# Kernel optimization log

Measured on AMD Instinct MI355X. Metric: run time of the kernel, lower is better.

The kernel has to match this reference:

```python
import jax, jax.numpy as jnp
import numpy as np

G, M, K = 4096, 50, 30          # graphs, nodes per graph, sort-pool k
H, NUM_LAYERS, F_IN = 32, 3, 128
DEG = 8
N = G * M
E = N * DEG
D_LAT = H * NUM_LAYERS + 1       # 97 = conv1d kernel/stride
DENSE_DIM = (((K - 2) // 2 + 1) - 5 + 1) * 32  # 352


def setup_inputs() -> dict:
    key = jax.random.key(0)
    ks = jax.random.split(key, 14)
    x = jax.random.normal(ks[0], (N, F_IN), dtype=jnp.float32)
    # graph-local random edges so each subgraph is self-contained
    offs = (jnp.arange(E, dtype=jnp.int32) // (M * DEG)) * M
    src = jax.random.randint(ks[1], (E,), 0, M, dtype=jnp.int32) + offs
    dst = jax.random.randint(ks[2], (E,), 0, M, dtype=jnp.int32) + offs
    edge_index = jnp.stack([src, dst])
    batch = jnp.repeat(jnp.arange(G, dtype=jnp.int32), M)

    def lin(k, i, o):
        return (jax.random.normal(k, (i, o), dtype=jnp.float32) / np.sqrt(i)).astype(jnp.float32)

    W0, b0 = lin(ks[3], F_IN, H), jnp.zeros((H,), jnp.float32)
    W1, b1 = lin(ks[4], H, H), jnp.zeros((H,), jnp.float32)
    W2, b2 = lin(ks[5], H, H), jnp.zeros((H,), jnp.float32)
    W3, b3 = lin(ks[6], H, 1), jnp.zeros((1,), jnp.float32)
    C1w = (jax.random.normal(ks[7], (16, 1, D_LAT)) / np.sqrt(D_LAT)).astype(jnp.float32)
    C1b = jnp.zeros((16,), jnp.float32)
    C2w = (jax.random.normal(ks[8], (32, 16, 5)) / np.sqrt(16 * 5)).astype(jnp.float32)
    C2b = jnp.zeros((32,), jnp.float32)
    L1w, L1b = lin(ks[9], DENSE_DIM, 128), jnp.zeros((128,), jnp.float32)
    L2w, L2b = lin(ks[10], 128, 1), jnp.zeros((1,), jnp.float32)
    return {"x": x, "edge_index": edge_index, "batch": batch,
            "W0": W0, "b0": b0, "W1": W1, "b1": b1, "W2": W2, "b2": b2,
            "W3": W3, "b3": b3, "C1w": C1w, "C1b": C1b, "C2w": C2w, "C2b": C2b,
            "L1w": L1w, "L1b": L1b, "L2w": L2w, "L2b": L2b}


def _gcn_norm(edge_index, n):
    # add self loops, symmetric normalization (PyG GCNConv default)
    loop = jnp.arange(n, dtype=edge_index.dtype)
    src = jnp.concatenate([edge_index[0], loop])
    dst = jnp.concatenate([edge_index[1], loop])
    deg = jax.ops.segment_sum(jnp.ones_like(dst, dtype=jnp.float32), dst, num_segments=n)
    dinv = jnp.where(deg > 0, deg ** -0.5, 0.0)
    return src, dst, dinv[src] * dinv[dst]


def _gcn_conv(h, W, b, src, dst, norm, n):
    h = h @ W                                    # [N, out]
    msg = h[src] * norm[:, None]                 # gather + weight
    return jax.ops.segment_sum(msg, dst, num_segments=n) + b


def reference(x, edge_index, batch, W0, b0, W1, b1, W2, b2, W3, b3,
              C1w, C1b, C2w, C2b, L1w, L1b, L2w, L2b):
    n = x.shape[0]
    src, dst, norm = _gcn_norm(edge_index, n)
    h1 = jnp.tanh(_gcn_conv(x, W0, b0, src, dst, norm, n))
    h2 = jnp.tanh(_gcn_conv(h1, W1, b1, src, dst, norm, n))
    h3 = jnp.tanh(_gcn_conv(h2, W2, b2, src, dst, norm, n))
    h4 = jnp.tanh(_gcn_conv(h3, W3, b3, src, dst, norm, n))
    lat = jnp.concatenate([h1, h2, h3, h4], axis=-1)      # [N, 97]
    # global_sort_pool: graphs are contiguous equal-size blocks (batch = arange(G).repeat(M)),
    # sort nodes within each graph by last channel, descending, keep top K
    xd = lat.reshape(G, M, D_LAT)
    order = jnp.argsort(-xd[..., -1], axis=1)             # [G, M]
    xs = jnp.take_along_axis(xd, order[..., None], axis=1)[:, :K]  # [G, K, 97]
    # Conv1d(1,16,97,stride=97) on [G,1,K*97] == per-slot linear over the 97 latent dims
    z = jnp.einsum('gtd,cd->gct', xs, C1w[:, 0, :]) + C1b[None, :, None]  # [G,16,K]
    z = jax.nn.relu(z)
    z = z.reshape(G, 16, K // 2, 2).max(axis=-1)          # MaxPool1d(2,2) -> [G,16,15]
    z = jax.lax.conv_general_dilated(z, C2w, window_strides=(1,), padding='VALID',
                                     dimension_numbers=('NCH', 'OIH', 'NCH'))
    z = jax.nn.relu(z + C2b[None, :, None])               # [G,32,11]
    z = z.reshape(G, -1)                                  # [G,352]
    z = jax.nn.relu(z @ L1w + L1b)
    # dropout: eval mode (identity)
    return z @ L2w + L2b                                  # [G,1]
```

## Files before the change

kernel.cpp:

```cpp
#include <hip/hip_runtime.h>
#include <math.h>

#define NG 4096
#define M 50
#define KTOP 30
#define H 32
#define F_IN 128
#define EPG 400
#define PADE 552
#define E_TOTAL (NG * EPG)
#define DLAT 97
#define LATS 100
#define NTHREADS 256
#define WS_C1P 0
#define XH 64

__device__ __forceinline__ float fast_tanh(float x) {
    x = fminf(fmaxf(x, -15.f), 15.f);
    float e = __expf(2.f * x);
    return 1.f - 2.f / (e + 1.f);
}

__global__ void prep_kernel(const float* __restrict__ C1w, float* __restrict__ ws) {
    const int tid = blockIdx.x * blockDim.x + threadIdx.x;
    if (tid < 1600) {
        int c = tid / 100, d = tid - c * 100;
        ws[WS_C1P + tid] = (d < DLAT) ? C1w[c * DLAT + d] : 0.f;
    }
}

template <int KIN>
__device__ __forceinline__ void gcn_matmul_acc(const float* hin, int istride,
                                               const float* W,
                                               const int* rows, float* acc, int j) {
#pragma unroll 2
    for (int k4 = 0; k4 < KIN / 4; k4++) {
        const float w0 = W[(4 * k4 + 0) * H + j];
        const float w1 = W[(4 * k4 + 1) * H + j];
        const float w2 = W[(4 * k4 + 2) * H + j];
        const float w3 = W[(4 * k4 + 3) * H + j];
#pragma unroll
        for (int r = 0; r < 7; r++) {
            const float4 xv = *(const float4*)(hin + rows[r] * istride + 4 * k4);
            acc[r] += xv.x * w0 + xv.y * w1 + xv.z * w2 + xv.w * w3;
        }
    }
}

template <int KIN>
__device__ __forceinline__ void gcn_matmul(const float* hin, int istride,
                                           const float* W,
                                           float (*tb)[H], const float* dinv, int tid) {
    const int j = tid & 31, iset = tid >> 5;
    float acc[7];
    int rows[7];
#pragma unroll
    for (int r = 0; r < 7; r++) {
        acc[r] = 0.f;
        int i = iset + r * 8;
        rows[r] = (i >= M) ? (M - 1) : i;
    }
    gcn_matmul_acc<KIN>(hin, istride, W, rows, acc, j);
#pragma unroll
    for (int r = 0; r < 7; r++) {
        int i = iset + r * 8;
        if (i < M) tb[i][j] = acc[r] * dinv[i];
    }
}

__device__ __forceinline__ void gcn_agg(const float (*tbuf)[H], const float* __restrict__ b,
                                        float (*lat)[LATS], int col0,
                                        const float* dinv, const unsigned short* csr_off,
                                        const unsigned char* csr_src, int tid) {
    const int j = tid & 31, iset = tid >> 5;
    for (int i = iset; i < M; i += 8) {
        float acc = tbuf[i][j];
        int e0 = csr_off[i], e1 = csr_off[i + 1];
        for (int e = e0; e < e1; e += 4) {
            unsigned sp = *(const unsigned*)(csr_src + e);
            acc += tbuf[sp & 255][j];
            acc += tbuf[(sp >> 8) & 255][j];
            acc += tbuf[(sp >> 16) & 255][j];
            acc += tbuf[sp >> 24][j];
        }
        lat[i][col0 + j] = fast_tanh(acc * dinv[i] + b[j]);
    }
}

struct Post {
    float pbuf[16][15];
    union {
        struct { float z1[16][KTOP]; unsigned char ord[52]; } a;
        struct { float z2[352]; float red[256]; } b;
    } u;
};

__global__ __launch_bounds__(NTHREADS, 4)
void dgcnn_kernel(const float* __restrict__ x, const int* __restrict__ eidx,
                  const float* __restrict__ ws,
                  const float* __restrict__ W0, const float* __restrict__ b0,
                  const float* __restrict__ W1, const float* __restrict__ b1,
                  const float* __restrict__ W2, const float* __restrict__ b2,
                  const float* __restrict__ W3, const float* __restrict__ b3,
                  const float* __restrict__ C1b,
                  const float* __restrict__ C2w, const float* __restrict__ C2b,
                  const float* __restrict__ L1w, const float* __restrict__ L1b,
                  const float* __restrict__ L2w, const float* __restrict__ L2b,
                  float* __restrict__ out) {
    __shared__ __align__(16) union Big {
        struct { float xs[M][XH]; float w0h[XH][H]; } p1;
        float lat[M][LATS];
    } big;
    __shared__ __align__(16) union TP {
        float tbuf[M + 1][H];
        Post post;
    } tp;
    __shared__ __align__(16) union W12U {
        float w[2][H][H];
        float c2w[32 * 16 * 5];
    } w12u;
    __shared__ unsigned char csr_src[PADE];
    __shared__ unsigned short csr_off[M + 2];
    __shared__ int   degi[M];
    __shared__ float dinv[M];

    const int g = blockIdx.x;
    const int tid = threadIdx.x;
    const int nbase = g * M;
    const int ebase = g * EPG;

    {
        const float4* xg4 = (const float4*)(x + (size_t)nbase * F_IN);
        float4* xs4 = (float4*)big.p1.xs;
        for (int idx = tid; idx < M * XH / 4; idx += NTHREADS) {
            int i = idx >> 4, q = idx & 15;
            xs4[idx] = xg4[i * 32 + q];
        }
        float4* w0f = (float4*)big.p1.w0h;
        const float4* w0g = (const float4*)W0;
        for (int idx = tid; idx < 512; idx += NTHREADS)
            w0f[idx] = w0g[idx];
        float4* wf = (float4*)w12u.w;
        for (int idx = tid; idx < 512; idx += NTHREADS) {
            const float4* srcp = (idx < 256) ? ((const float4*)W1 + idx)
                                             : ((const float4*)W2 + (idx - 256));
            wf[idx] = *srcp;
        }
    }
    if (tid < M) degi[tid] = 1;
    for (int idx = tid; idx < PADE / 4; idx += NTHREADS)
        ((unsigned*)csr_src)[idx] = 0x32323232u;
    __syncthreads();
    for (int e = tid; e < EPG; e += NTHREADS) {
        int d = eidx[E_TOTAL + ebase + e] - nbase;
        atomicAdd(&degi[d], 1);
    }
    __syncthreads();
    if (tid < M) dinv[tid] = rsqrtf((float)degi[tid]);
    if (tid < 64) {
        int cnt  = (tid < M) ? (degi[tid] - 1) : 0;
        int cntp = (cnt + 3) & ~3;
        int incl = cntp;
#pragma unroll
        for (int off = 1; off < 64; off <<= 1) {
            int nv = __shfl_up(incl, off);
            if (tid >= off) incl += nv;
        }
        if (tid < M) {
            csr_off[tid] = (unsigned short)(incl - cntp);
            degi[tid] = incl - cntp;
        }
        if (tid == M - 1) csr_off[M] = (unsigned short)incl;
    }
    __syncthreads();
    const int j1 = tid & 31, iset1 = tid >> 5;
    float acc1[7];
    int rows1[7];
#pragma unroll
    for (int r = 0; r < 7; r++) {
        acc1[r] = 0.f;
        int i = iset1 + r * 8;
        rows1[r] = (i >= M) ? (M - 1) : i;
    }
    for (int e = tid; e < EPG; e += NTHREADS) {
        int s = eidx[ebase + e] - nbase;
        int d = eidx[E_TOTAL + ebase + e] - nbase;
        int pos = atomicAdd(&degi[d], 1);
        csr_src[pos] = (unsigned char)s;
    }
    gcn_matmul_acc<XH>(&big.p1.xs[0][0], XH, &big.p1.w0h[0][0], rows1, acc1, j1);
    __syncthreads();
    {
        const float4* xg4 = (const float4*)(x + (size_t)nbase * F_IN);
        float4* xs4 = (float4*)big.p1.xs;
        for (int idx = tid; idx < M * XH / 4; idx += NTHREADS) {
            int i = idx >> 4, q = idx & 15;
            xs4[idx] = xg4[i * 32 + 16 + q];
        }
        float4* w0f = (float4*)big.p1.w0h;
        const float4* w0g = (const float4*)(W0 + XH * H);
        for (int idx = tid; idx < 512; idx += NTHREADS)
            w0f[idx] = w0g[idx];
    }
    __syncthreads();
    gcn_matmul_acc<XH>(&big.p1.xs[0][0], XH, &big.p1.w0h[0][0], rows1, acc1, j1);
#pragma unroll
    for (int r = 0; r < 7; r++) {
        int i = iset1 + r * 8;
        if (i < M) tp.tbuf[i][j1] = acc1[r] * dinv[i];
    }
    if (tid < H) tp.tbuf[M][tid] = 0.f;
    __syncthreads();

    gcn_agg(tp.tbuf, b0, big.lat, 0, dinv, csr_off, csr_src, tid);
    for (int idx = tid; idx < 3 * M; idx += NTHREADS)
        big.lat[idx / 3][DLAT + idx % 3] = 0.f;
    __syncthreads();
    gcn_matmul<H>(&big.lat[0][0], LATS, &w12u.w[0][0][0], tp.tbuf, dinv, tid);
    __syncthreads();
    gcn_agg(tp.tbuf, b1, big.lat, 32, dinv, csr_off, csr_src, tid);
    __syncthreads();
    gcn_matmul<H>(&big.lat[0][32], LATS, &w12u.w[1][0][0], tp.tbuf, dinv, tid);
    __syncthreads();
    gcn_agg(tp.tbuf, b2, big.lat, 64, dinv, csr_off, csr_src, tid);
    {
        float4* cf = (float4*)w12u.c2w;
        const float4* cg = (const float4*)C2w;
        for (int idx = tid; idx < 640; idx += NTHREADS)
            cf[idx] = cg[idx];
    }
    __syncthreads();
    if (tid < M) {
        float acc = 0.f;
        for (int k = 0; k < H; k++) acc += big.lat[tid][64 + k] * W3[k];
        tp.tbuf[tid][0] = acc * dinv[tid];
    }
    __syncthreads();
    if (tid < M) {
        float acc = tp.tbuf[tid][0];
        int e0 = csr_off[tid], e1 = csr_off[tid + 1];
        for (int e = e0; e < e1; e += 4) {
            unsigned sp = *(const unsigned*)(csr_src + e);
            acc += tp.tbuf[sp & 255][0] + tp.tbuf[(sp >> 8) & 255][0]
                 + tp.tbuf[(sp >> 16) & 255][0] + tp.tbuf[sp >> 24][0];
        }
        big.lat[tid][96] = tanhf(acc * dinv[tid] + b3[0]);
    }
    __syncthreads();

    if (tid < M) {
        float v = big.lat[tid][96];
        int r = 0;
        for (int jj = 0; jj < M; jj++) {
            float vj = big.lat[jj][96];
            r += (vj > v) || (vj == v && jj < tid);
        }
        tp.post.u.a.ord[r] = (unsigned char)tid;
    }
    __syncthreads();

    for (int idx = tid; idx < 16 * KTOP; idx += NTHREADS) {
        int t = idx >> 4, c = idx & 15;
        const float4* row = (const float4*)big.lat[tp.post.u.a.ord[t]];
        const float4* cw  = (const float4*)(ws + WS_C1P + c * LATS);
        float acc = 0.f;
#pragma unroll 5
        for (int q = 0; q < LATS / 4; q++) {
            float4 rv = row[q], wv = cw[q];
            acc += rv.x * wv.x + rv.y * wv.y + rv.z * wv.z + rv.w * wv.w;
        }
        tp.post.u.a.z1[c][t] = fmaxf(acc + C1b[c], 0.f);
    }
    __syncthreads();

    for (int idx = tid; idx < 16 * 15; idx += NTHREADS) {
        int c = idx / 15, t = idx - c * 15;
        tp.post.pbuf[c][t] = fmaxf(tp.post.u.a.z1[c][2 * t],
                                   tp.post.u.a.z1[c][2 * t + 1]);
    }
    __syncthreads();

    for (int idx = tid; idx < 352; idx += NTHREADS) {
        int o = idx / 11, t = idx - o * 11;
        float acc = C2b[o];
        for (int i = 0; i < 16; i++) {
#pragma unroll
            for (int k = 0; k < 5; k++)
                acc += tp.post.pbuf[i][t + k] * w12u.c2w[(o * 16 + i) * 5 + k];
        }
        tp.post.u.b.z2[idx] = fmaxf(acc, 0.f);
    }
    __syncthreads();

    {
        int jj = tid & 127, half = tid >> 7;
        int f0 = half * 176;
        const float* Lp = L1w + (size_t)f0 * 128 + jj;
        const float* zp = tp.post.u.b.z2 + f0;
        float a0 = 0.f, a1 = 0.f, a2 = 0.f, a3 = 0.f;
#pragma unroll 2
        for (int f = 0; f < 176; f += 4) {
            a0 += zp[f]     * Lp[(f)     * 128];
            a1 += zp[f + 1] * Lp[(f + 1) * 128];
            a2 += zp[f + 2] * Lp[(f + 2) * 128];
            a3 += zp[f + 3] * Lp[(f + 3) * 128];
        }
        float acc = (a0 + a1) + (a2 + a3) + ((half == 0) ? L1b[jj] : 0.f);
        tp.post.u.b.red[tid] = acc;
    }
    __syncthreads();
    if (tid < 128)
        tp.post.u.b.red[tid] =
            fmaxf(tp.post.u.b.red[tid] + tp.post.u.b.red[tid + 128], 0.f)
            * L2w[tid];
    __syncthreads();
    if (tid < 64) {
        float v = tp.post.u.b.red[tid] + tp.post.u.b.red[tid + 64];
#pragma unroll
        for (int off = 32; off >= 1; off >>= 1)
            v += __shfl_down(v, off);
        if (tid == 0) out[g] = v + L2b[0];
    }
}

extern "C" void kernel_launch(void* const* d_in, const int* in_sizes, int n_in,
                              void* d_out, int out_size, void* d_ws, size_t ws_size,
                              hipStream_t stream) {
    const float* x    = (const float*)d_in[0];
    const int*   eidx = (const int*)d_in[1];
    float* ws = (float*)d_ws;
    prep_kernel<<<7, 256, 0, stream>>>((const float*)d_in[11], ws);
    dgcnn_kernel<<<NG, NTHREADS, 0, stream>>>(
        x, eidx, ws,
        (const float*)d_in[3],  (const float*)d_in[4],
        (const float*)d_in[5],  (const float*)d_in[6],
        (const float*)d_in[7],  (const float*)d_in[8],
        (const float*)d_in[9],  (const float*)d_in[10],
        (const float*)d_in[12],
        (const float*)d_in[13], (const float*)d_in[14],
        (const float*)d_in[15], (const float*)d_in[16],
        (const float*)d_in[17], (const float*)d_in[18],
        (float*)d_out);
}
```

Before: 361.4 us.

## Transpose GCN weights in LDS and use packed FP32 FMA for matmuls

Weights W0, W1 and W2 are now stored transposed in shared memory with padded strides, so each thread reads contiguous pairs of its output column. The inner products use v_pk_fma_f32 via inline asm, carrying two partial sums per row. The matmul regions also raise wave priority with s_setprio. Conv1 uses packed FMA and conv2 splits its accumulation into two chains. The intent is to halve FMA issue count and cut LDS load instructions, at the cost of more bank-sensitive transposed stores, an extra reduction, and changed summation order.

```diff
diff --git a/kernel.cpp b/kernel.cpp
--- a/kernel.cpp
+++ b/kernel.cpp
@@ -14,6 +14,16 @@
 #define NTHREADS 256
 #define WS_C1P 0
 #define XH 64
+#define W0TS 66
+#define W12TS 34
+
+typedef float f32x2 __attribute__((ext_vector_type(2)));
+
+__device__ __forceinline__ f32x2 pk_fma(f32x2 a, f32x2 b, f32x2 c) {
+    f32x2 d;
+    asm("v_pk_fma_f32 %0, %1, %2, %3" : "=v"(d) : "v"(a), "v"(b), "v"(c));
+    return d;
+}
 
 __device__ __forceinline__ float fast_tanh(float x) {
     x = fminf(fmaxf(x, -15.f), 15.f);
@@ -31,40 +41,41 @@
 
 template <int KIN>
 __device__ __forceinline__ void gcn_matmul_acc(const float* hin, int istride,
-                                               const float* W,
-                                               const int* rows, float* acc, int j) {
+                                               const float* wtj,
+                                               const int* rows, f32x2* acc2) {
 #pragma unroll 2
     for (int k4 = 0; k4 < KIN / 4; k4++) {
-        const float w0 = W[(4 * k4 + 0) * H + j];
-        const float w1 = W[(4 * k4 + 1) * H + j];
-        const float w2 = W[(4 * k4 + 2) * H + j];
-        const float w3 = W[(4 * k4 + 3) * H + j];
+        const f32x2 wA = *(const f32x2*)(wtj + 4 * k4);
+        const f32x2 wB = *(const f32x2*)(wtj + 4 * k4 + 2);
 #pragma unroll
         for (int r = 0; r < 7; r++) {
-            const float4 xv = *(const float4*)(hin + rows[r] * istride + 4 * k4);
-            acc[r] += xv.x * w0 + xv.y * w1 + xv.z * w2 + xv.w * w3;
+            const f32x2* xp = (const f32x2*)(hin + rows[r] * istride + 4 * k4);
+            acc2[r] = pk_fma(xp[0], wA, acc2[r]);
+            acc2[r] = pk_fma(xp[1], wB, acc2[r]);
         }
     }
 }
 
 template <int KIN>
 __device__ __forceinline__ void gcn_matmul(const float* hin, int istride,
-                                           const float* W,
+                                           const float* wtj,
                                            float (*tb)[H], const float* dinv, int tid) {
     const int j = tid & 31, iset = tid >> 5;
-    float acc[7];
+    f32x2 acc[7];
     int rows[7];
 #pragma unroll
     for (int r = 0; r < 7; r++) {
-        acc[r] = 0.f;
+        acc[r] = (f32x2){0.f, 0.f};
         int i = iset + r * 8;
         rows[r] = (i >= M) ? (M - 1) : i;
     }
-    gcn_matmul_acc<KIN>(hin, istride, W, rows, acc, j);
+    __builtin_amdgcn_s_setprio(1);
+    gcn_matmul_acc<KIN>(hin, istride, wtj, rows, acc);
+    __builtin_amdgcn_s_setprio(0);
 #pragma unroll
     for (int r = 0; r < 7; r++) {
         int i = iset + r * 8;
-        if (i < M) tb[i][j] = acc[r] * dinv[i];
+        if (i < M) tb[i][j] = (acc[r].x + acc[r].y) * dinv[i];
     }
 }
 
@@ -108,7 +119,7 @@
                   const float* __restrict__ L2w, const float* __restrict__ L2b,
                   float* __restrict__ out) {
     __shared__ __align__(16) union Big {
-        struct { float xs[M][XH]; float w0h[XH][H]; } p1;
+        struct { float xs[M][XH]; float w0t[H][W0TS]; } p1;
         float lat[M][LATS];
     } big;
     __shared__ __align__(16) union TP {
@@ -116,7 +127,7 @@
         Post post;
     } tp;
     __shared__ __align__(16) union W12U {
-        float w[2][H][H];
+        float w[2][H][W12TS];
         float c2w[32 * 16 * 5];
     } w12u;
     __shared__ unsigned char csr_src[PADE];
@@ -136,15 +147,19 @@
             int i = idx >> 4, q = idx & 15;
             xs4[idx] = xg4[i * 32 + q];
         }
-        float4* w0f = (float4*)big.p1.w0h;
         const float4* w0g = (const float4*)W0;
-        for (int idx = tid; idx < 512; idx += NTHREADS)
-            w0f[idx] = w0g[idx];
-        float4* wf = (float4*)w12u.w;
         for (int idx = tid; idx < 512; idx += NTHREADS) {
-            const float4* srcp = (idx < 256) ? ((const float4*)W1 + idx)
-                                             : ((const float4*)W2 + (idx - 256));
-            wf[idx] = *srcp;
+            int k = idx >> 3, q4 = (idx & 7) * 4;
+            float4 v = w0g[idx];
+            big.p1.w0t[q4 + 0][k] = v.x; big.p1.w0t[q4 + 1][k] = v.y;
+            big.p1.w0t[q4 + 2][k] = v.z; big.p1.w0t[q4 + 3][k] = v.w;
+        }
+        for (int idx = tid; idx < 512; idx += NTHREADS) {
+            int m = idx >> 8, r = idx & 255;
+            int k = r >> 3, q4 = (r & 7) * 4;
+            float4 v = ((const float4*)(m ? W2 : W1))[r];
+            w12u.w[m][q4 + 0][k] = v.x; w12u.w[m][q4 + 1][k] = v.y;
+            w12u.w[m][q4 + 2][k] = v.z; w12u.w[m][q4 + 3][k] = v.w;
         }
     }
     if (tid < M) degi[tid] = 1;
@@ -174,11 +189,12 @@
     }
     __syncthreads();
     const int j1 = tid & 31, iset1 = tid >> 5;
-    float acc1[7];
+    const float* w0tj = &big.p1.w0t[j1][0];
+    f32x2 acc1[7];
     int rows1[7];
 #pragma unroll
     for (int r = 0; r < 7; r++) {
-        acc1[r] = 0.f;
+        acc1[r] = (f32x2){0.f, 0.f};
         int i = iset1 + r * 8;
         rows1[r] = (i >= M) ? (M - 1) : i;
     }
@@ -188,7 +204,9 @@
         int pos = atomicAdd(&degi[d], 1);
         csr_src[pos] = (unsigned char)s;
     }
-    gcn_matmul_acc<XH>(&big.p1.xs[0][0], XH, &big.p1.w0h[0][0], rows1, acc1, j1);
+    __builtin_amdgcn_s_setprio(1);
+    gcn_matmul_acc<XH>(&big.p1.xs[0][0], XH, w0tj, rows1, acc1);
+    __builtin_amdgcn_s_setprio(0);
     __syncthreads();
     {
         const float4* xg4 = (const float4*)(x + (size_t)nbase * F_IN);
@@ -197,17 +215,22 @@
             int i = idx >> 4, q = idx & 15;
             xs4[idx] = xg4[i * 32 + 16 + q];
         }
-        float4* w0f = (float4*)big.p1.w0h;
         const float4* w0g = (const float4*)(W0 + XH * H);
-        for (int idx = tid; idx < 512; idx += NTHREADS)
-            w0f[idx] = w0g[idx];
-    }
-    __syncthreads();
-    gcn_matmul_acc<XH>(&big.p1.xs[0][0], XH, &big.p1.w0h[0][0], rows1, acc1, j1);
+        for (int idx = tid; idx < 512; idx += NTHREADS) {
+            int k = idx >> 3, q4 = (idx & 7) * 4;
+            float4 v = w0g[idx];
+            big.p1.w0t[q4 + 0][k] = v.x; big.p1.w0t[q4 + 1][k] = v.y;
+            big.p1.w0t[q4 + 2][k] = v.z; big.p1.w0t[q4 + 3][k] = v.w;
+        }
+    }
+    __syncthreads();
+    __builtin_amdgcn_s_setprio(1);
+    gcn_matmul_acc<XH>(&big.p1.xs[0][0], XH, w0tj, rows1, acc1);
+    __builtin_amdgcn_s_setprio(0);
 #pragma unroll
     for (int r = 0; r < 7; r++) {
         int i = iset1 + r * 8;
-        if (i < M) tp.tbuf[i][j1] = acc1[r] * dinv[i];
+        if (i < M) tp.tbuf[i][j1] = (acc1[r].x + acc1[r].y) * dinv[i];
     }
     if (tid < H) tp.tbuf[M][tid] = 0.f;
     __syncthreads();
@@ -216,11 +239,11 @@
     for (int idx = tid; idx < 3 * M; idx += NTHREADS)
         big.lat[idx / 3][DLAT + idx % 3] = 0.f;
     __syncthreads();
-    gcn_matmul<H>(&big.lat[0][0], LATS, &w12u.w[0][0][0], tp.tbuf, dinv, tid);
+    gcn_matmul<H>(&big.lat[0][0], LATS, &w12u.w[0][tid & 31][0], tp.tbuf, dinv, tid);
     __syncthreads();
     gcn_agg(tp.tbuf, b1, big.lat, 32, dinv, csr_off, csr_src, tid);
     __syncthreads();
-    gcn_matmul<H>(&big.lat[0][32], LATS, &w12u.w[1][0][0], tp.tbuf, dinv, tid);
+    gcn_matmul<H>(&big.lat[0][32], LATS, &w12u.w[1][tid & 31][0], tp.tbuf, dinv, tid);
     __syncthreads();
     gcn_agg(tp.tbuf, b2, big.lat, 64, dinv, csr_off, csr_src, tid);
     {
@@ -261,14 +284,15 @@
 
     for (int idx = tid; idx < 16 * KTOP; idx += NTHREADS) {
         int t = idx >> 4, c = idx & 15;
-        const float4* row = (const float4*)big.lat[tp.post.u.a.ord[t]];
-        const float4* cw  = (const float4*)(ws + WS_C1P + c * LATS);
-        float acc = 0.f;
+        const f32x2* row2 = (const f32x2*)big.lat[tp.post.u.a.ord[t]];
+        const f32x2* cw2  = (const f32x2*)(ws + WS_C1P + c * LATS);
+        f32x2 a01 = (f32x2){0.f, 0.f}, a23 = (f32x2){0.f, 0.f};
 #pragma unroll 5
         for (int q = 0; q < LATS / 4; q++) {
-            float4 rv = row[q], wv = cw[q];
-            acc += rv.x * wv.x + rv.y * wv.y + rv.z * wv.z + rv.w * wv.w;
-        }
+            a01 = pk_fma(row2[2 * q],     cw2[2 * q],     a01);
+            a23 = pk_fma(row2[2 * q + 1], cw2[2 * q + 1], a23);
+        }
+        float acc = (a01.x + a01.y) + (a23.x + a23.y);
         tp.post.u.a.z1[c][t] = fmaxf(acc + C1b[c], 0.f);
     }
     __syncthreads();
@@ -282,13 +306,15 @@
 
     for (int idx = tid; idx < 352; idx += NTHREADS) {
         int o = idx / 11, t = idx - o * 11;
-        float acc = C2b[o];
-        for (int i = 0; i < 16; i++) {
-#pragma unroll
-            for (int k = 0; k < 5; k++)
-                acc += tp.post.pbuf[i][t + k] * w12u.c2w[(o * 16 + i) * 5 + k];
-        }
-        tp.post.u.b.z2[idx] = fmaxf(acc, 0.f);
+        float a0 = C2b[o], a1 = 0.f;
+        for (int i = 0; i < 16; i += 2) {
+#pragma unroll
+            for (int k = 0; k < 5; k++) {
+                a0 += tp.post.pbuf[i][t + k]     * w12u.c2w[(o * 16 + i) * 5 + k];
+                a1 += tp.post.pbuf[i + 1][t + k] * w12u.c2w[(o * 16 + i + 1) * 5 + k];
+            }
+        }
+        tp.post.u.b.z2[idx] = fmaxf(a0 + a1, 0.f);
     }
     __syncthreads();
 
```

After: 394.4 us. +9.1%, slower.
